# Kernel tuning notes

Hardware: AMD Instinct MI355X
Metric: run time of the kernel (lower is better)

## Reference

```python
import jax, jax.numpy as jnp
import numpy as np

T, B, E, H, V = 50, 64, 1024, 1024, 32000
NL = 2


def setup_inputs() -> dict:
    key = jax.random.key(0)
    ks = jax.random.split(key, 16)
    def rn(k, shape, fan_in):
        return jax.random.normal(k, shape, jnp.float32) * (1.0 / np.sqrt(fan_in))
    return {
        "word": jax.random.randint(ks[0], (B,), 0, V),
        "seq": jax.random.randint(ks[1], (T, B), 0, V),
        "emb": jax.random.normal(ks[2], (V, E), jnp.float32) * 0.05,
        "w2h_W": rn(ks[3], (H, E), E),
        "w2h_b": jnp.zeros((H,), jnp.float32),
        "W_ih0": rn(ks[4], (4 * H, 2 * E), 2 * E),
        "W_hh0": rn(ks[5], (4 * H, H), H),
        "b_ih0": jnp.zeros((4 * H,), jnp.float32),
        "b_hh0": jnp.zeros((4 * H,), jnp.float32),
        "W_ih1": rn(ks[6], (4 * H, H), H),
        "W_hh1": rn(ks[7], (4 * H, H), H),
        "b_ih1": jnp.zeros((4 * H,), jnp.float32),
        "b_hh1": jnp.zeros((4 * H,), jnp.float32),
        "dec_W": rn(ks[8], (V, H), H),
        "dec_b": jnp.zeros((V,), jnp.float32),
    }


def _lstm_layer(x, Wih, Whh, bih, bhh, h0, c0):
    """x: [T,B,D] -> hs: [T,B,H]. PyTorch gate order: i,f,g,o."""
    b = bih + bhh
    # precompute input contribution for all timesteps (one big GEMM)
    xg = jnp.einsum('tbd,gd->tbg', x, Wih) + b  # [T,B,4H]

    def step(carry, xt):
        h, c = carry
        gates = xt + h @ Whh.T
        i, f, g, o = jnp.split(gates, 4, axis=-1)
        c = jax.nn.sigmoid(f) * c + jax.nn.sigmoid(i) * jnp.tanh(g)
        h = jax.nn.sigmoid(o) * jnp.tanh(c)
        return (h, c), h

    (hT, cT), hs = jax.lax.scan(step, (h0, c0), xg)
    return hs, hT, cT


def reference(word, seq, emb, w2h_W, w2h_b, W_ih0, W_hh0, b_ih0, b_hh0,
              W_ih1, W_hh1, b_ih1, b_hh1, dec_W, dec_b):
    word_emb = emb[word]            # [B,E]
    seq_emb = emb[seq]              # [T,B,E]
    # init_hidden: c = word2hidden(word_emb) expanded over layers, h = zeros
    c0 = word_emb @ w2h_W.T + w2h_b          # [B,H]
    h0 = jnp.zeros_like(c0)
    # use_input: concat word_emb to every timestep input
    x0 = jnp.concatenate(
        [jnp.broadcast_to(word_emb[None], (T, B, E)), seq_emb], axis=-1)  # [T,B,2E]
    hs0, h0T, c0T = _lstm_layer(x0, W_ih0, W_hh0, b_ih0, b_hh0, h0, c0)
    hs1, h1T, c1T = _lstm_layer(hs0, W_ih1, W_hh1, b_ih1, b_hh1, h0, c0)
    outputs = hs1.reshape(T * B, H)
    decoded = outputs @ dec_W.T + dec_b      # [T*B, V]
    h_final = jnp.stack([h0T, h1T], 0)       # [NL,B,H]
    c_final = jnp.stack([c0T, c1T], 0)
    return decoded, h_final, c_final
```

## Files before the change

kernel.cpp:

```cpp
#include <hip/hip_runtime.h>
#include <cstddef>


static constexpr int T_ = 50, B_ = 64, E_ = 1024, H_ = 1024, V_ = 32000;
static constexpr int G_ = 4096;

typedef unsigned short u16;
typedef unsigned int u32;
typedef unsigned long long u64;
typedef __attribute__((ext_vector_type(8))) short bf16x8;
typedef __attribute__((ext_vector_type(8))) unsigned short u16x8;
typedef __attribute__((ext_vector_type(4))) float f32x4;

__device__ __forceinline__ int perm_g(int n) {
  return ((n >> 4) & 3) * H_ + (n >> 6) * 16 + (n & 15);
}
__device__ __forceinline__ u16 bf16_rn(float x) {
  union { float f; unsigned u; } a; a.f = x;
  unsigned r = a.u + 0x7fffu + ((a.u >> 16) & 1u);
  return (u16)(r >> 16);
}
__device__ __forceinline__ float bf16_f(u16 h) {
  union { float f; unsigned u; } a; a.u = ((unsigned)h) << 16;
  return a.f;
}
__device__ __forceinline__ float sigm(float x) { return 1.f / (1.f + __expf(-x)); }

__global__ void fill_zero(float* p, int n) {
  int i = blockIdx.x * blockDim.x + threadIdx.x;
  if (i < n) p[i] = 0.f;
}
__global__ void bias_perm(const float* a, const float* b, float* dst) {
  int n = blockIdx.x * 256 + threadIdx.x;
  int s = perm_g(n);
  dst[n] = a[s] + b[s];
}

__global__ void conv_w(const float* __restrict__ src, int srcld, int coloff,
                       const int* __restrict__ gidx, int PERM, int rows,
                       u16* __restrict__ dst) {
  int idx = blockIdx.x * 256 + threadIdx.x;
  int r = idx >> 7, kc = (idx & 127) << 3;
  if (r >= rows) return;
  int s = gidx ? gidx[r] : (PERM ? perm_g(r) : r);
  const float* p = src + (size_t)s * srcld + coloff + kc;
  float4 v0 = *(const float4*)p, v1 = *(const float4*)(p + 4);
  float vv[8] = {v0.x, v0.y, v0.z, v0.w, v1.x, v1.y, v1.z, v1.w};
  u16 hi[8], lo[8];
#pragma unroll
  for (int i = 0; i < 8; ++i) {
    hi[i] = bf16_rn(vv[i]);
    lo[i] = bf16_rn(vv[i] - bf16_f(hi[i]));
  }
  u16x8 c0, c1;
#pragma unroll
  for (int i = 0; i < 4; ++i) {
    c0[2 * i] = hi[i];     c0[2 * i + 1] = lo[i];
    c1[2 * i] = hi[4 + i]; c1[2 * i + 1] = lo[4 + i];
  }
  int seg = kc >> 5;
  int ch0 = (kc >> 2) & 7;
  size_t base = (size_t)r * 2048 + seg * 64;
  *(u16x8*)&dst[base + (size_t)((ch0 ^ (r & 7)) << 3)] = c0;
  *(u16x8*)&dst[base + (size_t)(((ch0 | 1) ^ (r & 7)) << 3)] = c1;
}

template<int BM, int BN, int BK, int TM, int TN>
__launch_bounds__(256)
__global__ void gemm_nt(
    const float* __restrict__ A, const int* __restrict__ Aidx, int lda,
    const float* __restrict__ W, int ldw, int koff,
    const float* __restrict__ bias, float* __restrict__ C, float* __restrict__ C2,
    int ldc, int M, int N, int K) {
  constexpr int TX = BN / TN;
  constexpr int TY = BM / TM;
  static_assert(TX * TY == 256, "thread geometry");
  __shared__ float As[BK][BM + 4];
  __shared__ float Ws[BK][BN + 4];
  const int tid = threadIdx.x;
  const int tx = tid % TX, ty = tid / TX;
  const int m0 = blockIdx.y * BM, n0 = blockIdx.x * BN;
  float acc[TM][TN];
#pragma unroll
  for (int i = 0; i < TM; ++i)
#pragma unroll
    for (int j = 0; j < TN; ++j) acc[i][j] = 0.f;
  constexpr int AV = (BM * BK) / 4;
  constexpr int WV = (BN * BK) / 4;
  constexpr int KV = BK / 4;
  for (int k0 = 0; k0 < K; k0 += BK) {
#pragma unroll
    for (int lp = 0; lp < (AV + 255) / 256; ++lp) {
      int e = tid + lp * 256;
      if (e < AV) {
        int r = e / KV, kq = e % KV;
        int m = m0 + r;
        float4 v = make_float4(0.f, 0.f, 0.f, 0.f);
        if (m < M) {
          int row = Aidx ? Aidx[m] : m;
          v = *(const float4*)&A[(size_t)row * lda + k0 + kq * 4];
        }
        As[kq * 4 + 0][r] = v.x; As[kq * 4 + 1][r] = v.y;
        As[kq * 4 + 2][r] = v.z; As[kq * 4 + 3][r] = v.w;
      }
    }
#pragma unroll
    for (int lp = 0; lp < (WV + 255) / 256; ++lp) {
      int e = tid + lp * 256;
      if (e < WV) {
        int cc = e / KV, kq = e % KV;
        int n = n0 + cc;
        float4 v = make_float4(0.f, 0.f, 0.f, 0.f);
        if (n < N)
          v = *(const float4*)&W[(size_t)n * ldw + koff + k0 + kq * 4];
        Ws[kq * 4 + 0][cc] = v.x; Ws[kq * 4 + 1][cc] = v.y;
        Ws[kq * 4 + 2][cc] = v.z; Ws[kq * 4 + 3][cc] = v.w;
      }
    }
    __syncthreads();
#pragma unroll
    for (int kk = 0; kk < BK; ++kk) {
      float a[TM], b[TN];
#pragma unroll
      for (int i = 0; i < TM; ++i) a[i] = As[kk][ty * TM + i];
#pragma unroll
      for (int j = 0; j < TN; ++j) b[j] = Ws[kk][tx * TN + j];
#pragma unroll
      for (int i = 0; i < TM; ++i)
#pragma unroll
        for (int j = 0; j < TN; ++j)
          acc[i][j] += a[i] * b[j];
    }
    __syncthreads();
  }
#pragma unroll
  for (int i = 0; i < TM; ++i) {
    int m = m0 + ty * TM + i;
    if (m >= M) continue;
#pragma unroll
    for (int j = 0; j < TN; ++j) {
      int n = n0 + tx * TN + j;
      if (n >= N) continue;
      float v = acc[i][j];
      if (bias) v += bias[n];
      C[(size_t)m * ldc + n] = v;
      if (C2) C2[(size_t)m * ldc + n] = v;
    }
  }
}

__launch_bounds__(256)
__global__ void gemm_bt(const u16* __restrict__ A, int Mrows,
                        const u16* __restrict__ Wb,
                        const float* __restrict__ bias,
                        const float* __restrict__ Dadd, int ldd, int dmask,
                        float* __restrict__ C, int ldc, int N, int nbx,
                        int mt, int ord) {
  __shared__ u16 lsA[128 * 64];
  __shared__ u16 lsB[128 * 64];

  int nwg = gridDim.x, bid = blockIdx.x;
  int q = nwg >> 3, r = nwg & 7;
  int xcd = bid & 7, base = bid >> 3;
  int wg = (xcd < r ? xcd * (q + 1) : r * (q + 1) + (xcd - r) * q) + base;
  int bx, by;
  if (ord) { by = wg % mt; bx = wg / mt; } else { bx = wg % nbx; by = wg / nbx; }
  const int m0 = by * 128, n0 = bx * 128;

  const int tid = threadIdx.x, w = tid >> 6, l = tid & 63;
  const int lr = l & 15, lq = l >> 4;
  const int wm = (w >> 1) * 64, wn = (w & 1) * 64;

  f32x4 acc[4][4] = {};

  for (int kt = 0; kt < 32; ++kt) {
#pragma unroll
    for (int i = 0; i < 4; ++i) {
      int rb = w * 32 + i * 8;
      int gm = m0 + rb + (l >> 3);
      if (gm > Mrows - 1) gm = Mrows - 1;
      const u16* ga = A + (size_t)gm * 2048 + kt * 64 + (l & 7) * 8;
      __builtin_amdgcn_global_load_lds(
          (const __attribute__((address_space(1))) void*)ga,
          (__attribute__((address_space(3))) void*)(lsA + rb * 64), 16, 0, 0);
      const u16* gb = Wb + (size_t)(n0 + rb + (l >> 3)) * 2048 + kt * 64 + (l & 7) * 8;
      __builtin_amdgcn_global_load_lds(
          (const __attribute__((address_space(1))) void*)gb,
          (__attribute__((address_space(3))) void*)(lsB + rb * 64), 16, 0, 0);
    }
    asm volatile("s_waitcnt vmcnt(0)" ::: "memory");
    __syncthreads();

    bf16x8 af[4][2], bfr[4][2];
#pragma unroll
    for (int i = 0; i < 4; ++i) {
      int ar = wm + i * 16 + lr;
#pragma unroll
      for (int s = 0; s < 2; ++s)
        af[i][s] = *(const bf16x8*)&lsA[ar * 64 + (((s << 2) + lq) ^ (ar & 7)) * 8];
    }
#pragma unroll
    for (int j = 0; j < 4; ++j) {
      int br = wn + j * 16 + lr;
#pragma unroll
      for (int s = 0; s < 2; ++s)
        bfr[j][s] = *(const bf16x8*)&lsB[br * 64 + (((s << 2) + lq) ^ (br & 7)) * 8];
    }
#pragma unroll
    for (int i = 0; i < 4; ++i)
#pragma unroll
      for (int j = 0; j < 4; ++j) {
        acc[i][j] = __builtin_amdgcn_mfma_f32_16x16x32_bf16(af[i][0], bfr[j][0], acc[i][j], 0, 0, 0);
        acc[i][j] = __builtin_amdgcn_mfma_f32_16x16x32_bf16(af[i][1], bfr[j][1], acc[i][j], 0, 0, 0);
      }
    __syncthreads();
  }

#pragma unroll
  for (int i = 0; i < 4; ++i) {
    int mbase = m0 + wm + i * 16 + lq * 4;
#pragma unroll
    for (int j = 0; j < 4; ++j) {
      int n = n0 + wn + j * 16 + lr;
      float badd = bias ? bias[n] : 0.f;
#pragma unroll
      for (int rr = 0; rr < 4; ++rr) {
        int m = mbase + rr;
        if (m >= Mrows) continue;
        float v = acc[i][j][rr] + badd;
        if (Dadd) {
          int dr = (dmask < 0) ? m : (m & dmask);
          v += Dadd[(size_t)dr * ldd + n];
        }
        C[(size_t)m * ldc + n] = v;
      }
    }
  }
}

__launch_bounds__(256)
__global__ void gemm_sp(
    const float* __restrict__ A, int lda,
    const float* __restrict__ W, int ldw,
    const float* __restrict__ bias,
    float* __restrict__ C, int ldc, int M, int N, int K, int nbx) {
  __shared__ u16 As_h[128][40], As_l[128][40];
  __shared__ u16 Ws_h[128][40], Ws_l[128][40];
  int nwg = gridDim.x, bid = blockIdx.x;
  int q = nwg >> 3, r = nwg & 7;
  int xcd = bid & 7, base = bid >> 3;
  int wg = (xcd < r ? xcd * (q + 1) : r * (q + 1) + (xcd - r) * q) + base;
  int bx = wg % nbx, by = wg / nbx;
  const int m0 = by * 128, n0 = bx * 128;
  const int tid = threadIdx.x;
  const int wave = tid >> 6, lane = tid & 63;
  const int lr = lane & 15, lq = lane >> 4;
  const int wm = (wave >> 1) * 64, wn = (wave & 1) * 64;
  f32x4 acc[4][4] = {};
  for (int k0 = 0; k0 < K; k0 += 32) {
#pragma unroll
    for (int lp = 0; lp < 4; ++lp) {
      int s = tid + lp * 256;
      int row = s >> 3, kq = s & 7;
      float4 v = make_float4(0.f, 0.f, 0.f, 0.f);
      int gm = m0 + row;
      if (gm < M)
        v = *(const float4*)&A[(size_t)gm * lda + k0 + kq * 4];
      u16 h0 = bf16_rn(v.x), h1 = bf16_rn(v.y), h2 = bf16_rn(v.z), h3 = bf16_rn(v.w);
      u16 l0 = bf16_rn(v.x - bf16_f(h0)), l1 = bf16_rn(v.y - bf16_f(h1));
      u16 l2 = bf16_rn(v.z - bf16_f(h2)), l3 = bf16_rn(v.w - bf16_f(h3));
      *(uint2*)&As_h[row][kq * 4] =
          make_uint2((u32)h0 | ((u32)h1 << 16), (u32)h2 | ((u32)h3 << 16));
      *(uint2*)&As_l[row][kq * 4] =
          make_uint2((u32)l0 | ((u32)l1 << 16), (u32)l2 | ((u32)l3 << 16));
    }
#pragma unroll
    for (int lp = 0; lp < 4; ++lp) {
      int s = tid + lp * 256;
      int col = s >> 3, kq = s & 7;
      int n = n0 + col;
      float4 v = make_float4(0.f, 0.f, 0.f, 0.f);
      if (n < N)
        v = *(const float4*)&W[(size_t)n * ldw + k0 + kq * 4];
      u16 h0 = bf16_rn(v.x), h1 = bf16_rn(v.y), h2 = bf16_rn(v.z), h3 = bf16_rn(v.w);
      u16 l0 = bf16_rn(v.x - bf16_f(h0)), l1 = bf16_rn(v.y - bf16_f(h1));
      u16 l2 = bf16_rn(v.z - bf16_f(h2)), l3 = bf16_rn(v.w - bf16_f(h3));
      *(uint2*)&Ws_h[col][kq * 4] =
          make_uint2((u32)h0 | ((u32)h1 << 16), (u32)h2 | ((u32)h3 << 16));
      *(uint2*)&Ws_l[col][kq * 4] =
          make_uint2((u32)l0 | ((u32)l1 << 16), (u32)l2 | ((u32)l3 << 16));
    }
    __syncthreads();
    bf16x8 ah[4], al[4], bh[4], bl[4];
#pragma unroll
    for (int i = 0; i < 4; ++i) {
      ah[i] = *(const bf16x8*)&As_h[wm + i * 16 + lr][lq * 8];
      al[i] = *(const bf16x8*)&As_l[wm + i * 16 + lr][lq * 8];
    }
#pragma unroll
    for (int j = 0; j < 4; ++j) {
      bh[j] = *(const bf16x8*)&Ws_h[wn + j * 16 + lr][lq * 8];
      bl[j] = *(const bf16x8*)&Ws_l[wn + j * 16 + lr][lq * 8];
    }
#pragma unroll
    for (int i = 0; i < 4; ++i)
#pragma unroll
      for (int j = 0; j < 4; ++j) {
        acc[i][j] = __builtin_amdgcn_mfma_f32_16x16x32_bf16(ah[i], bh[j], acc[i][j], 0, 0, 0);
        acc[i][j] = __builtin_amdgcn_mfma_f32_16x16x32_bf16(ah[i], bl[j], acc[i][j], 0, 0, 0);
        acc[i][j] = __builtin_amdgcn_mfma_f32_16x16x32_bf16(al[i], bh[j], acc[i][j], 0, 0, 0);
      }
    __syncthreads();
  }
#pragma unroll
  for (int i = 0; i < 4; ++i) {
    int mbase = m0 + wm + i * 16 + lq * 4;
#pragma unroll
    for (int j = 0; j < 4; ++j) {
      int n = n0 + wn + j * 16 + lr;
      if (n >= N) continue;
      float badd = bias ? bias[n] : 0.f;
#pragma unroll
      for (int rr = 0; rr < 4; ++rr) {
        int m = mbase + rr;
        if (m >= M) continue;
        C[(size_t)m * ldc + n] = acc[i][j][rr] + badd;
      }
    }
  }
}

__device__ __forceinline__ void gemm_half(
    const u32* __restrict__ hp, int rg, int w, int lr, int lq,
    const bf16x8 (&bfr)[8][4], f32x4 (&acc)[2][4]) {
  bf16x8 af[8][2];
#pragma unroll
  for (int s = 0; s < 8; ++s)
#pragma unroll
    for (int mt = 0; mt < 2; ++mt) {
      int m = rg * 32 + mt * 16 + lr;
      int seg = w * 4 + (s >> 1);
      int cis = ((((s & 1) << 2) + lq) ^ (lr & 7));
      const u32* p = hp + (size_t)m * 1024 + seg * 32 + cis * 4;
      asm volatile("global_load_dwordx4 %0, %1, off sc0 sc1"
                   : "=v"(af[s][mt]) : "v"(p) : "memory");
    }
  asm volatile("s_waitcnt vmcnt(0)" ::: "memory");
  __builtin_amdgcn_sched_barrier(0);
#pragma unroll
  for (int s = 0; s < 8; ++s)
#pragma unroll
    for (int mt = 0; mt < 2; ++mt)
#pragma unroll
      for (int nt = 0; nt < 4; ++nt)
        acc[mt][nt] = __builtin_amdgcn_mfma_f32_16x16x32_bf16(
            af[s][mt], bfr[s][nt], acc[mt][nt], 0, 0, 0);
}

__device__ __forceinline__ void poll_src(const u32* flags, int rg, int w, int l, u32 tgt) {
  int guard = 0;
  for (;;) {
    u32 v = tgt;
    if (l < 8)
      v = __hip_atomic_load(flags + (size_t)((rg << 6) + (w << 3) + l) * 4,
                            __ATOMIC_RELAXED, __HIP_MEMORY_SCOPE_AGENT);
    if (__all(v >= tgt)) break;
    if (++guard > (1 << 23)) break;
    __builtin_amdgcn_s_sleep(1);
  }
}

template<bool DUAL, bool EMIT>
__launch_bounds__(512, 1)
__global__ void rnn_dual(const u16* __restrict__ Whh0b, const u16* __restrict__ Whh1b,
                         const u16* __restrict__ Wih1b,
                         const float* __restrict__ xg0all, const float* __restrict__ bias1p,
                         float* __restrict__ cL0, float* __restrict__ hL0,
                         float* __restrict__ cL1, float* __restrict__ hL1,
                         u32* __restrict__ h0s, u32* __restrict__ h1s,
                         float* __restrict__ hsf,
                         u32* __restrict__ flg0, u32* __restrict__ flg1, int T) {
  __shared__ float partial[8][32][68];

  const int bid = blockIdx.x;
  const int x = bid & 7, j = bid >> 3;
  const int layer = DUAL ? (j & 1) : 0;
  const int idx = DUAL ? (j >> 1) : j;
  const int ct = x * 8 + (idx & 7);
  const int rg = idx >> 3;
  const int tid = threadIdx.x, w = tid >> 6, l = tid & 63;
  const int lr = l & 15, lq = l >> 4;

  const u16* WbA = (layer ? Whh1b : Whh0b) + (size_t)(ct * 64) * 2048;
  bf16x8 bfragA[8][4];
#pragma unroll
  for (int s = 0; s < 8; ++s)
#pragma unroll
    for (int nt = 0; nt < 4; ++nt) {
      int row = nt * 16 + lr;
      int seg = w * 4 + (s >> 1);
      int cis = ((((s & 1) << 2) + lq) ^ (lr & 7));
      bfragA[s][nt] = *(const bf16x8*)&WbA[(size_t)row * 2048 + seg * 64 + cis * 8];
    }
  bf16x8 bfragX[8][4];
  if (DUAL && layer) {
    const u16* WbX = Wih1b + (size_t)(ct * 64) * 2048;
#pragma unroll
    for (int s = 0; s < 8; ++s)
#pragma unroll
      for (int nt = 0; nt < 4; ++nt) {
        int row = nt * 16 + lr;
        int seg = w * 4 + (s >> 1);
        int cis = ((((s & 1) << 2) + lq) ^ (lr & 7));
        bfragX[s][nt] = *(const bf16x8*)&WbX[(size_t)row * 2048 + seg * 64 + cis * 8];
      }
  }

  const int cm = tid >> 4, cu = tid & 15;
  const int m_c = rg * 32 + cm;
  const int unit = ct * 16 + cu;
  float* cL = layer ? cL1 : cL0;
  float* hL = layer ? hL1 : hL0;
  u32* hsl = layer ? h1s : h0s;
  u32* flgS = layer ? flg1 : flg0;
  float creg = cL[m_c * H_ + unit];
  float bset[4];
  if (layer) {
#pragma unroll
    for (int g = 0; g < 4; ++g)
      bset[g] = bias1p[ct * 64 + g * 16 + cu];
  }

  for (int t = 0; t < T; ++t) {
    float xgv[4];
    if (!layer) {
      const float* xg = xg0all + (size_t)t * ((size_t)B_ * G_);
#pragma unroll
      for (int g = 0; g < 4; ++g)
        xgv[g] = xg[(size_t)m_c * G_ + ct * 64 + g * 16 + cu];
    } else {
#pragma unroll
      for (int g = 0; g < 4; ++g) xgv[g] = bset[g];
    }

    f32x4 acc[2][4] = {};

    if (layer) {
      if (t) poll_src(flg1, rg, w, l, (u32)t);
      gemm_half(h1s + (size_t)t * (B_ * 1024), rg, w, lr, lq, bfragA, acc);
      poll_src(flg0, rg, w, l, (u32)(t + 1));
      gemm_half(h0s + (size_t)(t + 1) * (B_ * 1024), rg, w, lr, lq, bfragX, acc);
    } else {
      if (t) poll_src(flg0, rg, w, l, (u32)t);
      gemm_half(h0s + (size_t)t * (B_ * 1024), rg, w, lr, lq, bfragA, acc);
    }

#pragma unroll
    for (int mt = 0; mt < 2; ++mt)
#pragma unroll
      for (int nt = 0; nt < 4; ++nt)
#pragma unroll
        for (int rr = 0; rr < 4; ++rr)
          partial[w][mt * 16 + lq * 4 + rr][nt * 16 + lr] = acc[mt][nt][rr];
    __syncthreads();

    float g4[4];
#pragma unroll
    for (int g = 0; g < 4; ++g) {
      float ssum = xgv[g];
#pragma unroll
      for (int p = 0; p < 8; ++p) ssum += partial[p][cm][g * 16 + cu];
      g4[g] = ssum;
    }
    float cn = sigm(g4[1]) * creg + sigm(g4[0]) * tanhf(g4[2]);
    float hn = sigm(g4[3]) * tanhf(cn);
    creg = cn;
    if (EMIT && layer) hsf[(size_t)t * (B_ * H_) + m_c * H_ + unit] = hn;
    if (t == T - 1) { cL[m_c * H_ + unit] = cn; hL[m_c * H_ + unit] = hn; }
    u16 hh = bf16_rn(hn);
    u16 hl2 = bf16_rn(hn - bf16_f(hh));
    u32 packed = (u32)hh | ((u32)hl2 << 16);
    u32* hnext = hsl + (size_t)(t + 1) * (B_ * 1024);
    u32 hidx = m_c * 1024 + ((unit >> 5) << 5) +
               ((((unit >> 2) & 7) ^ (m_c & 7)) << 2) + (unit & 3);
    {
      u32* sp = hnext + hidx;
      asm volatile("global_store_dword %0, %1, off sc0 sc1"
                   :: "v"(sp), "v"(packed) : "memory");
    }

    if (!layer || t < T - 1) {
      asm volatile("s_waitcnt vmcnt(0)" ::: "memory");
      __syncthreads();
      if (tid == 0)
        __hip_atomic_store(flgS + (size_t)((rg << 6) + ct) * 4, (u32)(t + 1),
                           __ATOMIC_RELAXED, __HIP_MEMORY_SCOPE_AGENT);
    }
  }
}

__launch_bounds__(256)
__global__ void rnn_step(const u16* __restrict__ hprev, const u16* __restrict__ Wb,
                         const float* __restrict__ xg,
                         float* __restrict__ c, float* __restrict__ hf,
                         u32* __restrict__ hout) {
  __shared__ char smem[32768];
  u16* lsA = (u16*)smem;
  u16* lsB = (u16*)(smem + 16384);
  const int nt = blockIdx.x, n0 = nt * 64;
  const int tid = threadIdx.x, w = tid >> 6, l = tid & 63;
  const int lr = l & 15, lq = l >> 4;
  f32x4 acc[4] = {};
  for (int kt = 0; kt < 16; ++kt) {
#pragma unroll
    for (int i = 0; i < 4; ++i) {
      int rb = w * 16 + i * 4;
      const u16* ga = hprev + (size_t)(rb + (l >> 4)) * 2048 + kt * 128 + (l & 15) * 8;
      __builtin_amdgcn_global_load_lds(
          (const __attribute__((address_space(1))) void*)ga,
          (__attribute__((address_space(3))) void*)(lsA + rb * 128), 16, 0, 0);
      const u16* gb = Wb + (size_t)(n0 + rb + (l >> 4)) * 2048 + kt * 128 + (l & 15) * 8;
      __builtin_amdgcn_global_load_lds(
          (const __attribute__((address_space(1))) void*)gb,
          (__attribute__((address_space(3))) void*)(lsB + rb * 128), 16, 0, 0);
    }
    asm volatile("s_waitcnt vmcnt(0)" ::: "memory");
    __syncthreads();
    bf16x8 af[4];
    int ar = w * 16 + lr;
#pragma unroll
    for (int s = 0; s < 4; ++s)
      af[s] = *(const bf16x8*)&lsA[ar * 128 + (s >> 1) * 64 + ((((s & 1) << 2) + lq) ^ (ar & 7)) * 8];
#pragma unroll
    for (int jj = 0; jj < 4; ++jj) {
      int br = jj * 16 + lr;
#pragma unroll
      for (int s = 0; s < 4; ++s) {
        bf16x8 bv = *(const bf16x8*)&lsB[br * 128 + (s >> 1) * 64 + ((((s & 1) << 2) + lq) ^ (br & 7)) * 8];
        acc[jj] = __builtin_amdgcn_mfma_f32_16x16x32_bf16(af[s], bv, acc[jj], 0, 0, 0);
      }
    }
    __syncthreads();
  }
  float* gsh = (float*)smem;
#pragma unroll
  for (int jj = 0; jj < 4; ++jj)
#pragma unroll
    for (int rr = 0; rr < 4; ++rr)
      gsh[(w * 16 + lq * 4 + rr) * 68 + jj * 16 + lr] = acc[jj][rr];
  __syncthreads();
  const int ui = tid & 15, mq = tid >> 4;
#pragma unroll
  for (int mr = 0; mr < 4; ++mr) {
    int m = mr * 16 + mq;
    float gi = gsh[m * 68 + 0 + ui]  + xg[(size_t)m * G_ + n0 + 0 + ui];
    float gf = gsh[m * 68 + 16 + ui] + xg[(size_t)m * G_ + n0 + 16 + ui];
    float gg = gsh[m * 68 + 32 + ui] + xg[(size_t)m * G_ + n0 + 32 + ui];
    float go = gsh[m * 68 + 48 + ui] + xg[(size_t)m * G_ + n0 + 48 + ui];
    int unit = nt * 16 + ui;
    int ci = m * H_ + unit;
    float cn = sigm(gf) * c[ci] + sigm(gi) * tanhf(gg);
    float hn = sigm(go) * tanhf(cn);
    c[ci] = cn;
    hf[ci] = hn;
    u16 hh = bf16_rn(hn);
    u16 hl = bf16_rn(hn - bf16_f(hh));
    u32 hidx = m * 1024 + ((unit >> 5) << 5) +
               ((((unit >> 2) & 7) ^ (m & 7)) << 2) + (unit & 3);
    hout[hidx] = (u32)hh | ((u32)hl << 16);
  }
}

extern "C" void kernel_launch(void* const* d_in, const int* in_sizes, int n_in,
                              void* d_out, int out_size, void* d_ws, size_t ws_size,
                              hipStream_t stream) {
  const int*   word  = (const int*)  d_in[0];
  const int*   seq   = (const int*)  d_in[1];
  const float* emb   = (const float*)d_in[2];
  const float* w2h_W = (const float*)d_in[3];
  const float* w2h_b = (const float*)d_in[4];
  const float* W_ih0 = (const float*)d_in[5];
  const float* W_hh0 = (const float*)d_in[6];
  const float* b_ih0 = (const float*)d_in[7];
  const float* b_hh0 = (const float*)d_in[8];
  const float* W_ih1 = (const float*)d_in[9];
  const float* W_hh1 = (const float*)d_in[10];
  const float* b_ih1 = (const float*)d_in[11];
  const float* b_hh1 = (const float*)d_in[12];
  const float* dec_W = (const float*)d_in[13];
  const float* dec_b = (const float*)d_in[14];

  float* out = (float*)d_out;
  float* hL0 = out + 102400000;
  float* hL1 = hL0 + B_ * H_;
  float* cL0 = out + 102531072;
  float* cL1 = cL0 + B_ * H_;

  float* xg0      = out;
  u16*   x0w_bf   = (u16*)(out + 13200000);
  u16*   x0seq_bf = (u16*)(out + 13300000);
  u32*   hs0slots = (u32*)(out + 16600000);
  u16*   wih0a_bf = (u16*)(out + 20000000);
  u16*   wih0b_bf = (u16*)(out + 24200000);
  u16*   wih1_bf  = (u16*)(out + 28400000);
  u16*   whh0_bf  = (u16*)(out + 32600000);
  u16*   whh1_bf  = (u16*)(out + 36800000);
  float* y_w      = out + 73800000;
  float* bias0p   = out + 74400000;
  float* bias1p   = out + 74410000;
  float* xg1      = out + 87560192;
  u32*   h1alt    = (u32*)(out + 91000000);
  u32*   flg0     = (u32*)(out + 101000000);
  u32*   flg1     = (u32*)(out + 101004096);
  u32*   hbfA     = (u32*)(out + 101100000);
  u32*   hbfB     = (u32*)(out + 101200000);

  const size_t need_hs1  = (size_t)T_ * B_ * H_ * 4;
  const size_t need_full = (size_t)V_ * 2048 * 2 + (size_t)(T_ + 1) * B_ * 1024 * 4;
  const bool tier1 = ws_size >= need_full;
  const bool tier2 = !tier1 && ws_size >= need_hs1;

  u16*   decW_bf  = (u16*)d_ws;
  u32*   hs1slots = (u32*)d_ws + (size_t)V_ * 1024;
  float* hs1f     = (float*)d_ws;

  fill_zero<<<32, 256, 0, stream>>>(out + 101000000, 8192);
  fill_zero<<<256, 256, 0, stream>>>((float*)hs0slots, 65536);
  if (tier1) fill_zero<<<256, 256, 0, stream>>>((float*)hs1slots, 65536);
  else if (tier2) fill_zero<<<256, 256, 0, stream>>>((float*)h1alt, 65536);
  bias_perm<<<16, 256, 0, stream>>>(b_ih0, b_hh0, bias0p);
  bias_perm<<<16, 256, 0, stream>>>(b_ih1, b_hh1, bias1p);

  gemm_nt<64, 64, 16, 4, 4><<<dim3(16, 1), 256, 0, stream>>>(
      emb, word, E_, w2h_W, E_, 0, w2h_b, cL0, cL1, H_, B_, H_, E_);

  conv_w<<<2048, 256, 0, stream>>>(W_ih0, 2 * E_, 0,  nullptr, 1, G_, wih0a_bf);
  conv_w<<<2048, 256, 0, stream>>>(W_ih0, 2 * E_, E_, nullptr, 1, G_, wih0b_bf);
  conv_w<<<2048, 256, 0, stream>>>(W_ih1, H_, 0, nullptr, 1, G_, wih1_bf);
  conv_w<<<2048, 256, 0, stream>>>(W_hh0, H_, 0, nullptr, 1, G_, whh0_bf);
  conv_w<<<2048, 256, 0, stream>>>(W_hh1, H_, 0, nullptr, 1, G_, whh1_bf);
  conv_w<<<32,   256, 0, stream>>>(emb, E_, 0, word, 0, B_, x0w_bf);
  conv_w<<<1600, 256, 0, stream>>>(emb, E_, 0, seq, 0, T_ * B_, x0seq_bf);
  if (tier1)
    conv_w<<<16000, 256, 0, stream>>>(dec_W, H_, 0, nullptr, 0, V_, decW_bf);

  gemm_bt<<<32, 256, 0, stream>>>(x0w_bf, B_, wih0a_bf, bias0p,
                                  nullptr, 0, -1, y_w, G_, G_, 32, 1, 0);
  gemm_bt<<<800, 256, 0, stream>>>(x0seq_bf, T_ * B_, wih0b_bf, nullptr,
                                   y_w, G_, 63, xg0, G_, G_, 32, 25, 0);

  if (tier1) {
    rnn_dual<true, false><<<256, 512, 0, stream>>>(
        whh0_bf, whh1_bf, wih1_bf, xg0, bias1p,
        cL0, hL0, cL1, hL1, hs0slots, hs1slots, nullptr, flg0, flg1, T_);
    gemm_bt<<<6250, 256, 0, stream>>>((const u16*)(hs1slots + (size_t)B_ * 1024),
                                      T_ * B_, decW_bf, dec_b,
                                      nullptr, 0, -1, out, V_, V_, 250, 25, 1);
  } else if (tier2) {
    rnn_dual<true, true><<<256, 512, 0, stream>>>(
        whh0_bf, whh1_bf, wih1_bf, xg0, bias1p,
        cL0, hL0, cL1, hL1, hs0slots, h1alt, hs1f, flg0, flg1, T_);
    gemm_sp<<<6250, 256, 0, stream>>>(
        hs1f, H_, dec_W, H_, dec_b, out, V_, T_ * B_, V_, H_, 250);
  } else {
    rnn_dual<false, false><<<128, 512, 0, stream>>>(
        whh0_bf, whh1_bf, wih1_bf, xg0, bias1p,
        cL0, hL0, cL1, hL1, hs0slots, nullptr, nullptr, flg0, flg1, T_);
    gemm_bt<<<800, 256, 0, stream>>>((const u16*)(hs0slots + (size_t)B_ * 1024),
                                     T_ * B_, wih1_bf, bias1p,
                                     nullptr, 0, -1, xg1, G_, G_, 32, 25, 0);
    for (int t = 0; t < T_; ++t) {
      const u16* hp = t ? (const u16*)((t & 1) ? hbfA : hbfB) : (const u16*)hs0slots;
      u32* ho = (t & 1) ? hbfB : hbfA;
      rnn_step<<<64, 256, 0, stream>>>(
          hp, whh1_bf, xg1 + (size_t)t * B_ * G_, cL1, hL1, ho);
      gemm_sp<<<250, 256, 0, stream>>>(
          hL1, H_, dec_W, H_, dec_b, out + (size_t)t * B_ * V_, V_, B_, V_, H_, 250);
    }
  }
}
```

Before: 1.770 ms.

## Overlap decoder weight conversion with recurrence and fuse setup kernels

The separate dec_W fp32-to-bf16 conversion launch is moved into extra blocks of the tier-1 recurrent kernel. Those blocks run alongside the latency-bound LSTM recurrence instead of before it. The five weight and two embedding conversion launches become one conv_all kernel, and the zero-fill and bias-permute launches become one init_all kernel, which cuts launch count. The risks are memory-bandwidth contention with the recurrence and the need for the extra blocks to coexist with the spin-waiting recurrent blocks; the flag buffer for layer 1 is also relocated.

```diff
diff --git a/kernel.cpp b/kernel.cpp
--- a/kernel.cpp
+++ b/kernel.cpp
@@ -36,10 +36,10 @@
   dst[n] = a[s] + b[s];
 }
 
-__global__ void conv_w(const float* __restrict__ src, int srcld, int coloff,
-                       const int* __restrict__ gidx, int PERM, int rows,
-                       u16* __restrict__ dst) {
-  int idx = blockIdx.x * 256 + threadIdx.x;
+__device__ __forceinline__ void conv_body(
+    const float* __restrict__ src, int srcld, int coloff,
+    const int* __restrict__ gidx, int PERM, int rows,
+    u16* __restrict__ dst, int idx) {
   int r = idx >> 7, kc = (idx & 127) << 3;
   if (r >= rows) return;
   int s = gidx ? gidx[r] : (PERM ? perm_g(r) : r);
@@ -63,6 +63,58 @@
   size_t base = (size_t)r * 2048 + seg * 64;
   *(u16x8*)&dst[base + (size_t)((ch0 ^ (r & 7)) << 3)] = c0;
   *(u16x8*)&dst[base + (size_t)(((ch0 | 1) ^ (r & 7)) << 3)] = c1;
+}
+
+__global__ void conv_w(const float* __restrict__ src, int srcld, int coloff,
+                       const int* __restrict__ gidx, int PERM, int rows,
+                       u16* __restrict__ dst) {
+  conv_body(src, srcld, coloff, gidx, PERM, rows, dst,
+            blockIdx.x * 256 + threadIdx.x);
+}
+
+__global__ void conv_all(const float* __restrict__ Wih0, const float* __restrict__ Wih1,
+                         const float* __restrict__ Whh0, const float* __restrict__ Whh1,
+                         const float* __restrict__ emb,
+                         const int* __restrict__ word, const int* __restrict__ seq,
+                         u16* wih0a, u16* wih0b, u16* wih1, u16* whh0, u16* whh1,
+                         u16* x0w, u16* x0seq) {
+  int b = blockIdx.x;
+  if (b < 2048)
+    conv_body(Wih0, 2048, 0, nullptr, 1, G_, wih0a, b * 256 + threadIdx.x);
+  else if (b < 4096)
+    conv_body(Wih0, 2048, 1024, nullptr, 1, G_, wih0b, (b - 2048) * 256 + threadIdx.x);
+  else if (b < 6144)
+    conv_body(Wih1, 1024, 0, nullptr, 1, G_, wih1, (b - 4096) * 256 + threadIdx.x);
+  else if (b < 8192)
+    conv_body(Whh0, 1024, 0, nullptr, 1, G_, whh0, (b - 6144) * 256 + threadIdx.x);
+  else if (b < 10240)
+    conv_body(Whh1, 1024, 0, nullptr, 1, G_, whh1, (b - 8192) * 256 + threadIdx.x);
+  else if (b < 10272)
+    conv_body(emb, 1024, 0, word, 0, B_, x0w, (b - 10240) * 256 + threadIdx.x);
+  else
+    conv_body(emb, 1024, 0, seq, 0, T_ * B_, x0seq, (b - 10272) * 256 + threadIdx.x);
+}
+
+__global__ void init_all(float* zf, float* z0, float* z1,
+                         const float* bi0, const float* bh0, float* b0p,
+                         const float* bi1, const float* bh1, float* b1p) {
+  int b = blockIdx.x, tid = threadIdx.x;
+  if (b < 32) {
+    int i = b * 256 + tid;
+    if (i < 8192) zf[i] = 0.f;
+  } else if (b < 288) {
+    z0[(b - 32) * 256 + tid] = 0.f;
+  } else if (b < 544) {
+    if (z1) z1[(b - 288) * 256 + tid] = 0.f;
+  } else if (b < 560) {
+    int n = (b - 544) * 256 + tid;
+    int s = perm_g(n);
+    b0p[n] = bi0[s] + bh0[s];
+  } else {
+    int n = (b - 560) * 256 + tid;
+    int s = perm_g(n);
+    b1p[n] = bi1[s] + bh1[s];
+  }
 }
 
 template<int BM, int BN, int BK, int TM, int TN>
@@ -370,7 +422,7 @@
   }
 }
 
-template<bool DUAL, bool EMIT>
+template<bool DUAL, bool EMIT, bool CONVW>
 __launch_bounds__(512, 1)
 __global__ void rnn_dual(const u16* __restrict__ Whh0b, const u16* __restrict__ Whh1b,
                          const u16* __restrict__ Wih1b,
@@ -379,17 +431,29 @@
                          float* __restrict__ cL1, float* __restrict__ hL1,
                          u32* __restrict__ h0s, u32* __restrict__ h1s,
                          float* __restrict__ hsf,
-                         u32* __restrict__ flg0, u32* __restrict__ flg1, int T) {
+                         u32* __restrict__ flg0, u32* __restrict__ flg1,
+                         const float* __restrict__ decW, u16* __restrict__ decWb,
+                         int T) {
   __shared__ float partial[8][32][68];
 
   const int bid = blockIdx.x;
+  const int tid = threadIdx.x, w = tid >> 6, l = tid & 63;
+  const int lr = l & 15, lq = l >> 4;
+
+  if (CONVW && bid >= 256) {
+    const int cb = bid - 256;
+    for (int it = 0; it < 125; ++it) {
+      int e = it * 512 + tid;
+      conv_body(decW, 1024, 0, nullptr, 0, V_, decWb, cb * 64000 + e);
+    }
+    return;
+  }
+
   const int x = bid & 7, j = bid >> 3;
   const int layer = DUAL ? (j & 1) : 0;
   const int idx = DUAL ? (j >> 1) : j;
   const int ct = x * 8 + (idx & 7);
   const int rg = idx >> 3;
-  const int tid = threadIdx.x, w = tid >> 6, l = tid & 63;
-  const int lr = l & 15, lq = l >> 4;
 
   const u16* WbA = (layer ? Whh1b : Whh0b) + (size_t)(ct * 64) * 2048;
   bf16x8 bfragA[8][4];
@@ -611,7 +675,6 @@
   float* xg1      = out + 87560192;
   u32*   h1alt    = (u32*)(out + 91000000);
   u32*   flg0     = (u32*)(out + 101000000);
-  u32*   flg1     = (u32*)(out + 101004096);
   u32*   hbfA     = (u32*)(out + 101100000);
   u32*   hbfB     = (u32*)(out + 101200000);
 
@@ -624,25 +687,17 @@
   u32*   hs1slots = (u32*)d_ws + (size_t)V_ * 1024;
   float* hs1f     = (float*)d_ws;
 
-  fill_zero<<<32, 256, 0, stream>>>(out + 101000000, 8192);
-  fill_zero<<<256, 256, 0, stream>>>((float*)hs0slots, 65536);
-  if (tier1) fill_zero<<<256, 256, 0, stream>>>((float*)hs1slots, 65536);
-  else if (tier2) fill_zero<<<256, 256, 0, stream>>>((float*)h1alt, 65536);
-  bias_perm<<<16, 256, 0, stream>>>(b_ih0, b_hh0, bias0p);
-  bias_perm<<<16, 256, 0, stream>>>(b_ih1, b_hh1, bias1p);
+  init_all<<<576, 256, 0, stream>>>(
+      out + 101000000, (float*)hs0slots,
+      tier1 ? (float*)hs1slots : (tier2 ? (float*)h1alt : nullptr),
+      b_ih0, b_hh0, bias0p, b_ih1, b_hh1, bias1p);
 
   gemm_nt<64, 64, 16, 4, 4><<<dim3(16, 1), 256, 0, stream>>>(
       emb, word, E_, w2h_W, E_, 0, w2h_b, cL0, cL1, H_, B_, H_, E_);
 
-  conv_w<<<2048, 256, 0, stream>>>(W_ih0, 2 * E_, 0,  nullptr, 1, G_, wih0a_bf);
-  conv_w<<<2048, 256, 0, stream>>>(W_ih0, 2 * E_, E_, nullptr, 1, G_, wih0b_bf);
-  conv_w<<<2048, 256, 0, stream>>>(W_ih1, H_, 0, nullptr, 1, G_, wih1_bf);
-  conv_w<<<2048, 256, 0, stream>>>(W_hh0, H_, 0, nullptr, 1, G_, whh0_bf);
-  conv_w<<<2048, 256, 0, stream>>>(W_hh1, H_, 0, nullptr, 1, G_, whh1_bf);
-  conv_w<<<32,   256, 0, stream>>>(emb, E_, 0, word, 0, B_, x0w_bf);
-  conv_w<<<1600, 256, 0, stream>>>(emb, E_, 0, seq, 0, T_ * B_, x0seq_bf);
-  if (tier1)
-    conv_w<<<16000, 256, 0, stream>>>(dec_W, H_, 0, nullptr, 0, V_, decW_bf);
+  conv_all<<<11872, 256, 0, stream>>>(
+      W_ih0, W_ih1, W_hh0, W_hh1, emb, word, seq,
+      wih0a_bf, wih0b_bf, wih1_bf, whh0_bf, whh1_bf, x0w_bf, x0seq_bf);
 
   gemm_bt<<<32, 256, 0, stream>>>(x0w_bf, B_, wih0a_bf, bias0p,
                                   nullptr, 0, -1, y_w, G_, G_, 32, 1, 0);
@@ -650,22 +705,25 @@
                                    y_w, G_, 63, xg0, G_, G_, 32, 25, 0);
 
   if (tier1) {
-    rnn_dual<true, false><<<256, 512, 0, stream>>>(
+    rnn_dual<true, false, true><<<320, 512, 0, stream>>>(
         whh0_bf, whh1_bf, wih1_bf, xg0, bias1p,
-        cL0, hL0, cL1, hL1, hs0slots, hs1slots, nullptr, flg0, flg1, T_);
+        cL0, hL0, cL1, hL1, hs0slots, hs1slots, nullptr, flg0, flg0 + 1024,
+        dec_W, decW_bf, T_);
     gemm_bt<<<6250, 256, 0, stream>>>((const u16*)(hs1slots + (size_t)B_ * 1024),
                                       T_ * B_, decW_bf, dec_b,
                                       nullptr, 0, -1, out, V_, V_, 250, 25, 1);
   } else if (tier2) {
-    rnn_dual<true, true><<<256, 512, 0, stream>>>(
+    rnn_dual<true, true, false><<<256, 512, 0, stream>>>(
         whh0_bf, whh1_bf, wih1_bf, xg0, bias1p,
-        cL0, hL0, cL1, hL1, hs0slots, h1alt, hs1f, flg0, flg1, T_);
+        cL0, hL0, cL1, hL1, hs0slots, h1alt, hs1f, flg0, flg0 + 1024,
+        nullptr, nullptr, T_);
     gemm_sp<<<6250, 256, 0, stream>>>(
         hs1f, H_, dec_W, H_, dec_b, out, V_, T_ * B_, V_, H_, 250);
   } else {
-    rnn_dual<false, false><<<128, 512, 0, stream>>>(
+    rnn_dual<false, false, false><<<128, 512, 0, stream>>>(
         whh0_bf, whh1_bf, wih1_bf, xg0, bias1p,
-        cL0, hL0, cL1, hL1, hs0slots, nullptr, nullptr, flg0, flg1, T_);
+        cL0, hL0, cL1, hL1, hs0slots, nullptr, nullptr, flg0, flg0 + 1024,
+        nullptr, nullptr, T_);
     gemm_bt<<<800, 256, 0, stream>>>((const u16*)(hs0slots + (size_t)B_ * 1024),
                                      T_ * B_, wih1_bf, bias1p,
                                      nullptr, 0, -1, xg1, G_, G_, 32, 25, 0);
```

New measurement: 1.806 ms. +2.0%, slower.
